# Performance work log

Measured on AMD Instinct MI355X. Metric: run time of the kernel, lower is better.

The kernel has to match this reference:

```python
import jax, jax.numpy as jnp
import numpy as np

DIM = 192; HEADS = 6; HD = DIM // HEADS; SCALE = HD ** -0.5
WS = (4, 8, 8); SS = (2, 4, 4)
NW = WS[0] * WS[1] * WS[2]  # tokens per window = 256
HIDDEN = 768; RANK1 = 384; RANK2 = 96

def _rel_index():
    Wd, Wh, Ww = WS
    coords = np.stack(np.meshgrid(np.arange(Wd), np.arange(Wh), np.arange(Ww), indexing='ij')).reshape(3, -1)
    rel = (coords[:, :, None] - coords[:, None, :]).transpose(1, 2, 0)
    rel = rel + np.array([Wd - 1, Wh - 1, Ww - 1])
    rel[:, :, 0] *= (2 * Wh - 1) * (2 * Ww - 1)
    rel[:, :, 1] *= 2 * Ww - 1
    return rel.sum(-1)  # (NW, NW) int

REL_IDX = jnp.asarray(_rel_index())

def _attn_mask(B, D, H, W):
    # static numpy computation (D,H,W are python ints) -> constant under jit
    img = np.zeros((B, D, H, W), np.float32); cnt = 0
    for d in range(0, D, WS[0]):
        for h in range(0, H, WS[1]):
            for w in range(0, W, WS[2]):
                img[:, d:d + WS[0], h:h + WS[1], w:w + WS[2]] = cnt; cnt += 1
    if any(s > 0 for s in SS):
        img = np.roll(img, (-SS[0], -SS[1], -SS[2]), axis=(1, 2, 3))
    mw = img.reshape(B, D // WS[0], WS[0], H // WS[1], WS[1], W // WS[2], WS[2]).transpose(0, 1, 3, 5, 2, 4, 6).reshape(-1, NW)
    diff = mw[:, :, None] - mw[:, None, :]
    return jnp.asarray(np.where(diff != 0, -100.0, 0.0).astype(np.float32))  # (B*nW, NW, NW)

def _ln(x, g, b):
    mu = x.mean(-1, keepdims=True)
    var = ((x - mu) ** 2).mean(-1, keepdims=True)
    return (x - mu) / jnp.sqrt(var + 1e-5) * g + b

def setup_inputs() -> dict:
    key = jax.random.key(0)
    ks = jax.random.split(key, 16)
    B, D, H, W = 1, 16, 64, 64
    N = D * H * W
    s = 0.02
    return {
        'x': jax.random.normal(ks[0], (B, N, DIM), jnp.float32),
        'norm1_g': jnp.ones((DIM,), jnp.float32), 'norm1_b': jnp.zeros((DIM,), jnp.float32),
        'qkv_w': jax.random.normal(ks[1], (DIM, 3 * DIM), jnp.float32) * s,
        'qkv_b': jnp.zeros((3 * DIM,), jnp.float32),
        'rel_bias': jax.random.normal(ks[2], (1575, HEADS), jnp.float32) * s,
        'proj_w': jax.random.normal(ks[3], (DIM, DIM), jnp.float32) * s,
        'proj_b': jnp.zeros((DIM,), jnp.float32),
        'norm2_g': jnp.ones((DIM,), jnp.float32), 'norm2_b': jnp.zeros((DIM,), jnp.float32),
        'fc1_A': jax.random.normal(ks[4], (DIM, RANK1), jnp.float32) * s,
        'fc1_Bw': jax.random.normal(ks[5], (RANK1, HIDDEN), jnp.float32) * s,
        'fc1_Bb': jnp.zeros((HIDDEN,), jnp.float32),
        'dw_w': jax.random.normal(ks[6], (HIDDEN, 1, 3, 3, 3), jnp.float32) * s,
        'dw_b': jnp.zeros((HIDDEN,), jnp.float32),
        'fc2_A': jax.random.normal(ks[7], (HIDDEN, RANK2), jnp.float32) * s,
        'fc2_Bw': jax.random.normal(ks[8], (RANK2, DIM), jnp.float32) * s,
        'fc2_Bb': jnp.zeros((DIM,), jnp.float32),
        'D': D, 'H': H, 'W': W,
    }

def reference(x, norm1_g, norm1_b, qkv_w, qkv_b, rel_bias, proj_w, proj_b,
              norm2_g, norm2_b, fc1_A, fc1_Bw, fc1_Bb, dw_w, dw_b,
              fc2_A, fc2_Bw, fc2_Bb, D, H, W):
    B, N, C = x.shape
    Wd, Wh, Ww = WS
    shortcut = x
    # --- shifted-window attention (NB: original repo never rolls x; only the mask is shifted) ---
    h = _ln(x, norm1_g, norm1_b).reshape(B, D, H, W, C)
    xw = h.reshape(B, D // Wd, Wd, H // Wh, Wh, W // Ww, Ww, C)
    xw = xw.transpose(0, 1, 3, 5, 2, 4, 6, 7).reshape(-1, NW, C)  # (B*nW, NW, C)
    qkv = (xw @ qkv_w + qkv_b).reshape(-1, NW, 3, HEADS, HD).transpose(2, 0, 3, 1, 4)
    q, k, v = qkv[0] * SCALE, qkv[1], qkv[2]           # (B*nW, heads, NW, hd)
    attn = jnp.einsum('bhnd,bhmd->bhnm', q, k)
    bias = rel_bias[REL_IDX].transpose(2, 0, 1)[None]  # (1, heads, NW, NW)
    mask = _attn_mask(B, D, H, W)                      # (B*nW, NW, NW)
    attn = jax.nn.softmax(attn + bias + mask[:, None], axis=-1)
    out = jnp.einsum('bhnm,bhmd->bhnd', attn, v).transpose(0, 2, 1, 3).reshape(-1, NW, C)
    out = out @ proj_w + proj_b
    out = out.reshape(B, D // Wd, H // Wh, W // Ww, Wd, Wh, Ww, C)
    out = out.transpose(0, 1, 4, 2, 5, 3, 6, 7).reshape(B, N, C)
    x = shortcut + out
    # --- MixFFN3D: low-rank fc1 -> depthwise conv3d -> GELU -> low-rank fc2 ---
    h = _ln(x, norm2_g, norm2_b)
    h = (h @ fc1_A) @ fc1_Bw + fc1_Bb                 # (B, N, HIDDEN)
    h = h.transpose(0, 2, 1).reshape(B, HIDDEN, D, H, W)
    h = jax.lax.conv_general_dilated(h, dw_w, (1, 1, 1), [(1, 1), (1, 1), (1, 1)],
                                     feature_group_count=HIDDEN,
                                     dimension_numbers=('NCDHW', 'OIDHW', 'NCDHW'))
    h = h + dw_b[None, :, None, None, None]
    h = jax.nn.gelu(h, approximate=False)
    h = h.reshape(B, HIDDEN, N).transpose(0, 2, 1)
    h = (h @ fc2_A) @ fc2_Bw + fc2_Bb                 # (B, N, DIM)
    return x + h
```

## Files before the change

kernel.cpp:

```cpp
#include <hip/hip_runtime.h>
#include <hip/hip_bf16.h>

typedef __hip_bfloat16 bf16;
typedef __attribute__((ext_vector_type(8))) short short8;
typedef __attribute__((ext_vector_type(4))) float f32x4;

#define N_TOK 65536
#define C_DIM 192
#define SCALE 0.17677669529663687f

__device__ __forceinline__ float b2f(bf16 v) { return __bfloat162float(v); }
__device__ __forceinline__ bf16 f2b(float v) { return __float2bfloat16(v); }
__device__ __forceinline__ float ldA(const void* p, size_t i, int f32) {
  return f32 ? ((const float*)p)[i] : b2f(((const bf16*)p)[i]);
}
__device__ __forceinline__ float s2f(short s) { union { short s; bf16 b; } u; u.s = s; return b2f(u.b); }

__device__ __forceinline__ float gelu_f(float s) {
  float t = s * s;
  float b = s * (-1.59576912f - 0.0713548162f * t);
  float e = __expf(b);
  return s / (1.f + e);
}

__global__ void detect_kernel(const unsigned short* __restrict__ xh, int* __restrict__ flag) {
  if (threadIdx.x == 0) {
    int crazy = 0;
    for (int i = 0; i < 256; ++i) {
      int e = (xh[i] >> 7) & 0xFF;
      if (e >= 0xF0 || (e >= 1 && e <= 0x60)) ++crazy;
    }
    *flag = (crazy >= 16) ? 1 : 0;
  }
}

__global__ __launch_bounds__(256) void prep_xpose_kernel(
    const void* __restrict__ qkv_w, bf16* __restrict__ QKVT,
    const void* __restrict__ proj_w, bf16* __restrict__ PROJT,
    const void* __restrict__ dw_w, bf16* __restrict__ DWT,
    const void* __restrict__ fc1_A, bf16* __restrict__ FC1AB,
    const void* __restrict__ fc1_Bw, bf16* __restrict__ FC1BWT,
    const void* __restrict__ fc2_A, bf16* __restrict__ FC2AB,
    const void* __restrict__ fc2_Bw, bf16* __restrict__ FC2BWT,
    const int* __restrict__ flag) {
  int f32 = *flag;
  int b = blockIdx.x;
  if (b < 432) {
    int idx = b * 256 + threadIdx.x;
    int n = idx / 192, k = idx - n * 192;
    QKVT[idx] = f2b(ldA(qkv_w, (size_t)k * 576 + n, f32));
  } else if (b < 576) {
    int idx = (b - 432) * 256 + threadIdx.x;
    int n = idx / 192, k = idx - n * 192;
    PROJT[idx] = f2b(ldA(proj_w, (size_t)k * 192 + n, f32));
  } else if (b < 657) {
    int idx = (b - 576) * 256 + threadIdx.x;
    int tap = idx / 768, c = idx - tap * 768;
    DWT[idx] = f2b(ldA(dw_w, (size_t)c * 27 + tap, f32));
  } else if (b < 945) {
    int idx = (b - 657) * 256 + threadIdx.x;
    FC1AB[idx] = f2b(ldA(fc1_A, idx, f32));
  } else if (b < 2097) {
    int idx = (b - 945) * 256 + threadIdx.x;
    int n = idx / 384, r = idx - n * 384;
    FC1BWT[idx] = f2b(ldA(fc1_Bw, (size_t)r * 768 + n, f32));
  } else if (b < 2385) {
    int idx = (b - 2097) * 256 + threadIdx.x;
    FC2AB[idx] = f2b(ldA(fc2_A, idx, f32));
  } else {
    int idx = (b - 2385) * 256 + threadIdx.x;
    int n = idx / 96, r = idx - n * 96;
    FC2BWT[idx] = f2b(ldA(fc2_Bw, (size_t)r * 192 + n, f32));
  }
}

__global__ __launch_bounds__(256) void ln_kernel(const void* __restrict__ x,
    const void* __restrict__ g, const void* __restrict__ b, bf16* __restrict__ out,
    int windowize, int xIsBf16Fixed, const int* __restrict__ flag) {
  int wf32 = *flag;
  int f32 = xIsBf16Fixed ? 0 : wf32;
  int token = blockIdx.x * 4 + (threadIdx.x >> 6);
  int lane = threadIdx.x & 63;
  size_t base = (size_t)token * C_DIM;
  float v0 = ldA(x, base + lane, f32);
  float v1 = ldA(x, base + lane + 64, f32);
  float v2 = ldA(x, base + lane + 128, f32);
  float s = v0 + v1 + v2;
  float s2 = v0 * v0 + v1 * v1 + v2 * v2;
  #pragma unroll
  for (int o = 32; o > 0; o >>= 1) { s += __shfl_xor(s, o, 64); s2 += __shfl_xor(s2, o, 64); }
  float mu = s * (1.f / 192.f);
  float var = s2 * (1.f / 192.f) - mu * mu;
  float rstd = rsqrtf(var + 1e-5f);
  int row = token;
  if (windowize) {
    int d = token >> 12, h = (token >> 6) & 63, w = token & 63;
    int win = ((d >> 2) << 6) + ((h >> 3) << 3) + (w >> 3);
    int t = ((d & 3) << 6) + ((h & 7) << 3) + (w & 7);
    row = win * 256 + t;
  }
  bf16* po = out + (size_t)row * C_DIM;
  po[lane]       = f2b((v0 - mu) * rstd * ldA(g, lane, wf32)       + ldA(b, lane, wf32));
  po[lane + 64]  = f2b((v1 - mu) * rstd * ldA(g, lane + 64, wf32)  + ldA(b, lane + 64, wf32));
  po[lane + 128] = f2b((v2 - mu) * rstd * ldA(g, lane + 128, wf32) + ldA(b, lane + 128, wf32));
}

__global__ __launch_bounds__(256) void mfma_gemm(const bf16* __restrict__ A,
    const bf16* __restrict__ BT, const void* __restrict__ bias,
    const void* __restrict__ res, void* __restrict__ out,
    int Nc, int K, int ldk, int mode, int Mrows, const int* __restrict__ flag) {
  int f32 = *flag;
  __shared__ short As[128 * 96];
  __shared__ short Bs[64 * 96];
  int tid = threadIdx.x;
  int wave = tid >> 6, lane = tid & 63;
  int wm = wave >> 1, wn = wave & 1;
  int lr = lane & 15, quad = lane >> 4;
  int rowBase, colBase;
  if (gridDim.y >= 8) {
    int ncb = gridDim.x;
    int flat = blockIdx.x + ncb * blockIdx.y;
    int group = flat / (8 * ncb);
    int r = flat - group * 8 * ncb;
    rowBase = (group * 8 + (r & 7)) * 128;
    colBase = (r >> 3) * 64;
  } else {
    rowBase = blockIdx.y * 128;
    colBase = blockIdx.x * 64;
  }
  f32x4 acc[4][2];
  #pragma unroll
  for (int i = 0; i < 4; ++i)
    #pragma unroll
    for (int j = 0; j < 2; ++j) acc[i][j] = f32x4{0.f, 0.f, 0.f, 0.f};

  const bf16* arow = A + (size_t)rowBase * K;
  const bf16* brow = BT + (size_t)colBase * ldk;

  for (int k0 = 0; k0 < K; k0 += 96) {
    #pragma unroll
    for (int it = 0; it < 6; ++it) {
      int u = tid + it * 256;
      int row = u / 12, kc = (u - row * 12) * 8;
      __builtin_amdgcn_global_load_lds(
          (const __attribute__((address_space(1))) void*)(arow + (size_t)row * K + k0 + kc),
          (__attribute__((address_space(3))) void*)&As[u * 8], 16, 0, 0);
    }
    #pragma unroll
    for (int it = 0; it < 3; ++it) {
      int u = tid + it * 256;
      int n = u / 12, kc = (u - n * 12) * 8;
      __builtin_amdgcn_global_load_lds(
          (const __attribute__((address_space(1))) void*)(brow + (size_t)n * ldk + k0 + kc),
          (__attribute__((address_space(3))) void*)&Bs[u * 8], 16, 0, 0);
    }
    __syncthreads();
    #pragma unroll
    for (int kk = 0; kk < 3; ++kk) {
      short8 af[4], bf[2];
      #pragma unroll
      for (int i = 0; i < 4; ++i)
        af[i] = *(const short8*)&As[(wm * 64 + i * 16 + lr) * 96 + kk * 32 + quad * 8];
      #pragma unroll
      for (int j = 0; j < 2; ++j)
        bf[j] = *(const short8*)&Bs[(wn * 32 + j * 16 + lr) * 96 + kk * 32 + quad * 8];
      #pragma unroll
      for (int i = 0; i < 4; ++i)
        #pragma unroll
        for (int j = 0; j < 2; ++j)
          acc[i][j] = __builtin_amdgcn_mfma_f32_16x16x32_bf16(af[i], bf[j], acc[i][j], 0, 0, 0);
    }
    __syncthreads();
  }

  #pragma unroll
  for (int i = 0; i < 4; ++i) {
    #pragma unroll
    for (int j = 0; j < 2; ++j) {
      #pragma unroll
      for (int r4 = 0; r4 < 4; ++r4) {
        int row = rowBase + wm * 64 + i * 16 + quad * 4 + r4;
        int c = colBase + wn * 32 + j * 16 + lr;
        if (c >= Nc || row >= Mrows) continue;
        float v = acc[i][j][r4];
        if (bias) v += ldA(bias, c, f32);
        if (mode == 0) {
          ((bf16*)out)[(size_t)row * Nc + c] = f2b(v);
        } else if (mode == 1) {
          float o = b2f(((const bf16*)res)[(size_t)row * Nc + c]) + v;
          if (f32) ((float*)out)[(size_t)row * Nc + c] = o;
          else     ((bf16*)out)[(size_t)row * Nc + c] = f2b(o);
        } else if (mode == 4) {
          ((bf16*)out)[(size_t)c * Mrows + row] = f2b(v);
        } else {
          int win = row >> 8, t = row & 255;
          int d = ((win >> 6) << 2) + (t >> 6);
          int h = (((win >> 3) & 7) << 3) + ((t >> 3) & 7);
          int w = ((win & 7) << 3) + (t & 7);
          int n = (d << 12) + (h << 6) + w;
          ((bf16*)out)[(size_t)n * C_DIM + c] = f2b(ldA(res, (size_t)n * C_DIM + c, f32) + v);
        }
      }
    }
  }
}

__global__ __launch_bounds__(256) void attn_mfma_kernel(const bf16* __restrict__ qkvr,
    const void* __restrict__ rel_bias, bf16* __restrict__ out,
    const int* __restrict__ flag) {
  int f32 = *flag;
  __shared__ bf16 sK[256 * 40];
  __shared__ bf16 sVT[32 * 264];
  __shared__ bf16 sP[4][64 * 40];
  __shared__ float sb[1575];
  __shared__ int  sgb[256];
  int head = blockIdx.x, win = blockIdx.y;
  const bf16* base = qkvr + (size_t)win * 256 * 576;
  int qoff = head * 32, koff = 192 + head * 32, voff = 384 + head * 32;
  int tid = threadIdx.x;
  int wave = tid >> 6, lane = tid & 63;
  int lr = lane & 15, quad = lane >> 4;

  #pragma unroll
  for (int it = 0; it < 4; ++it) {
    int idx = tid + it * 256;
    int tok = idx >> 2, kc = (idx & 3) * 8;
    uint4 v = *(const uint4*)(base + (size_t)tok * 576 + koff + kc);
    *(uint4*)&sK[tok * 40 + kc] = v;
  }
  for (int idx = tid; idx < 8192; idx += 256) {
    int tok = idx >> 5, hd = idx & 31;
    sVT[hd * 264 + tok] = base[(size_t)tok * 576 + voff + hd];
  }
  for (int idx = tid; idx < 1575; idx += 256) sb[idx] = ldA(rel_bias, (size_t)idx * 6 + head, f32);
  {
    int t = tid & 255;
    int d = ((win >> 6) << 2) + (t >> 6);
    int h = (((win >> 3) & 7) << 3) + ((t >> 3) & 7);
    int w = ((win & 7) << 3) + (t & 7);
    int d2 = (d + 2) & 15, h2 = (h + 4) & 63, w2 = (w + 4) & 63;
    int g = ((d2 >> 2) << 6) + ((h2 >> 3) << 3) + (w2 >> 3);
    int td = t >> 6, th = (t >> 3) & 7, tw = t & 7;
    int bse = (td * 15 + th) * 15 + tw;
    sgb[t] = (g << 12) | bse;
  }
  __syncthreads();

  int wm = wave * 64;
  short8 aq[4];
  #pragma unroll
  for (int i = 0; i < 4; ++i)
    aq[i] = *(const short8*)(base + (size_t)(wm + i * 16 + lr) * 576 + qoff + quad * 8);
  int rinfo[16];
  #pragma unroll
  for (int i = 0; i < 4; ++i)
    #pragma unroll
    for (int r = 0; r < 4; ++r)
      rinfo[i * 4 + r] = sgb[wm + i * 16 + quad * 4 + r];

  f32x4 acc_o[4][2], acc_l[4];
  #pragma unroll
  for (int i = 0; i < 4; ++i) {
    acc_l[i] = f32x4{0.f, 0.f, 0.f, 0.f};
    #pragma unroll
    for (int j = 0; j < 2; ++j) acc_o[i][j] = f32x4{0.f, 0.f, 0.f, 0.f};
  }
  short8 bones;
  #pragma unroll
  for (int j = 0; j < 8; ++j) bones[j] = (lr == 0) ? (short)0x3F80 : (short)0;

  for (int c = 0; c < 8; ++c) {
    short8 bk[2];
    #pragma unroll
    for (int jt = 0; jt < 2; ++jt)
      bk[jt] = *(const short8*)&sK[(c * 32 + jt * 16 + lr) * 40 + quad * 8];
    f32x4 s[4][2];
    #pragma unroll
    for (int i = 0; i < 4; ++i)
      #pragma unroll
      for (int jt = 0; jt < 2; ++jt) {
        s[i][jt] = f32x4{0.f, 0.f, 0.f, 0.f};
        s[i][jt] = __builtin_amdgcn_mfma_f32_16x16x32_bf16(aq[i], bk[jt], s[i][jt], 0, 0, 0);
      }
    int cinfo[2];
    #pragma unroll
    for (int jt = 0; jt < 2; ++jt) cinfo[jt] = sgb[c * 32 + jt * 16 + lr];
    #pragma unroll
    for (int i = 0; i < 4; ++i)
      #pragma unroll
      for (int jt = 0; jt < 2; ++jt)
        #pragma unroll
        for (int r = 0; r < 4; ++r) {
          int ri = rinfo[i * 4 + r], ci = cinfo[jt];
          float sc = s[i][jt][r] * SCALE + sb[(ri & 0xFFF) - (ci & 0xFFF) + 787];
          float p = ((ri >> 12) == (ci >> 12)) ? __expf(sc) : 0.f;
          sP[wave][(i * 16 + quad * 4 + r) * 40 + jt * 16 + lr] = f2b(p);
        }
    short8 ap[4];
    #pragma unroll
    for (int i = 0; i < 4; ++i)
      ap[i] = *(const short8*)&sP[wave][(i * 16 + lr) * 40 + quad * 8];
    short8 bv[2];
    #pragma unroll
    for (int jh = 0; jh < 2; ++jh)
      bv[jh] = *(const short8*)&sVT[(jh * 16 + lr) * 264 + c * 32 + quad * 8];
    #pragma unroll
    for (int i = 0; i < 4; ++i) {
      #pragma unroll
      for (int jh = 0; jh < 2; ++jh)
        acc_o[i][jh] = __builtin_amdgcn_mfma_f32_16x16x32_bf16(ap[i], bv[jh], acc_o[i][jh], 0, 0, 0);
      acc_l[i] = __builtin_amdgcn_mfma_f32_16x16x32_bf16(ap[i], bones, acc_l[i], 0, 0, 0);
    }
  }
  #pragma unroll
  for (int i = 0; i < 4; ++i) {
    #pragma unroll
    for (int r = 0; r < 4; ++r) {
      float l = __shfl(acc_l[i][r], lane & 48, 64);
      float inv = 1.f / l;
      int t = wm + i * 16 + quad * 4 + r;
      bf16* po = out + (size_t)(win * 256 + t) * C_DIM + head * 32;
      po[lr]      = f2b(acc_o[i][0][r] * inv);
      po[16 + lr] = f2b(acc_o[i][1][r] * inv);
    }
  }
}

__global__ __launch_bounds__(256) void dwconv8w4_kernel(const bf16* __restrict__ in,
    const bf16* __restrict__ wT, const void* __restrict__ wb, bf16* __restrict__ out,
    const int* __restrict__ flag) {
  int f32 = *flag;
  int idx = blockIdx.x * 256 + threadIdx.x;
  int n4 = idx / 96, g = idx - n4 * 96;
  int c0 = g * 8;
  int d = n4 >> 10, h = (n4 >> 4) & 63, w0 = (n4 & 15) << 2;
  const bf16* inb = in + c0;
  float acc[4][8];
  {
    float bias[8];
    #pragma unroll
    for (int e = 0; e < 8; ++e) bias[e] = ldA(wb, c0 + e, f32);
    #pragma unroll
    for (int t = 0; t < 4; ++t)
      #pragma unroll
      for (int e = 0; e < 8; ++e) acc[t][e] = bias[e];
  }
  #pragma unroll
  for (int kd = 0; kd < 3; ++kd) {
    int dd = d + kd - 1;
    if ((unsigned)dd >= 16u) continue;
    #pragma unroll
    for (int kh = 0; kh < 3; ++kh) {
      int hh = h + kh - 1;
      if ((unsigned)hh >= 64u) continue;
      int rowbase = (dd << 12) + (hh << 6);
      float xf[6][8];
      #pragma unroll
      for (int j = 0; j < 6; ++j) {
        int ww = w0 + j - 1;
        short8 xv = short8{0, 0, 0, 0, 0, 0, 0, 0};
        if ((unsigned)ww < 64u)
          xv = *(const short8*)(inb + (size_t)(rowbase + ww) * 768);
        #pragma unroll
        for (int e = 0; e < 8; ++e) xf[j][e] = s2f(xv[e]);
      }
      #pragma unroll
      for (int kw = 0; kw < 3; ++kw) {
        int tap = kd * 9 + kh * 3 + kw;
        short8 wv = *(const short8*)(wT + tap * 768 + c0);
        float wf[8];
        #pragma unroll
        for (int e = 0; e < 8; ++e) wf[e] = s2f(wv[e]);
        #pragma unroll
        for (int t = 0; t < 4; ++t)
          #pragma unroll
          for (int e = 0; e < 8; ++e)
            acc[t][e] += xf[t + kw][e] * wf[e];
      }
    }
  }
  #pragma unroll
  for (int t = 0; t < 4; ++t) {
    bf16* po = out + (size_t)((d << 12) + (h << 6) + w0 + t) * 768 + c0;
    #pragma unroll
    for (int e = 0; e < 8; ++e)
      po[e] = f2b(gelu_f(acc[t][e]));
  }
}

extern "C" void kernel_launch(void* const* d_in, const int* in_sizes, int n_in,
                              void* d_out, int out_size, void* d_ws, size_t ws_size,
                              hipStream_t stream) {
  const void* x      = d_in[0];
  const void* n1g    = d_in[1];
  const void* n1b    = d_in[2];
  const void* qkv_w  = d_in[3];
  const void* qkv_b  = d_in[4];
  const void* relb   = d_in[5];
  const void* proj_w = d_in[6];
  const void* proj_b = d_in[7];
  const void* n2g    = d_in[8];
  const void* n2b    = d_in[9];
  const void* fc1_A  = d_in[10];
  const void* fc1_Bw = d_in[11];
  const void* fc1_Bb = d_in[12];
  const void* dw_w   = d_in[13];
  const void* dw_b   = d_in[14];
  const void* fc2_A  = d_in[15];
  const void* fc2_Bw = d_in[16];
  const void* fc2_Bb = d_in[17];

  char* ws = (char*)d_ws;
  bf16* SCR  = (bf16*)d_out;
  bf16* X1   = (bf16*)(ws);
  bf16* QKVR = (bf16*)(ws + (size_t)24 * 1048576);
  bf16* F2   = (bf16*)(ws + (size_t)24 * 1048576);
  bf16* F1   = (bf16*)(ws + (size_t)120 * 1048576);
  bf16* QKVT   = (bf16*)(ws + (size_t)228 * 1048576);
  bf16* PROJT  = (bf16*)(ws + (size_t)229 * 1048576);
  bf16* DWT    = (bf16*)(ws + (size_t)230 * 1048576);
  bf16* W1T    = (bf16*)(ws + (size_t)231 * 1048576);
  bf16* W2T    = (bf16*)(ws + (size_t)232 * 1048576);
  bf16* FC1AB  = (bf16*)(ws + (size_t)233 * 1048576);
  bf16* FC1BWT = (bf16*)(ws + (size_t)234 * 1048576);
  bf16* FC2AB  = (bf16*)(ws + (size_t)236 * 1048576);
  bf16* FC2BWT = (bf16*)(ws + (size_t)237 * 1048576);
  int* FLAG    = (int*)(ws + (size_t)255 * 1048576);

  detect_kernel<<<1, 64, 0, stream>>>((const unsigned short*)x, FLAG);
  prep_xpose_kernel<<<2457, 256, 0, stream>>>(qkv_w, QKVT, proj_w, PROJT, dw_w, DWT,
                                              fc1_A, FC1AB, fc1_Bw, FC1BWT,
                                              fc2_A, FC2AB, fc2_Bw, FC2BWT, FLAG);
  mfma_gemm<<<dim3(12, 2), 256, 0, stream>>>(FC1AB, FC1BWT, nullptr, nullptr, W1T,
                                             768, 384, 384, 4, 192, FLAG);
  mfma_gemm<<<dim3(3, 6), 256, 0, stream>>>(FC2AB, FC2BWT, nullptr, nullptr, W2T,
                                            192, 96, 96, 4, 768, FLAG);
  ln_kernel<<<N_TOK / 4, 256, 0, stream>>>(x, n1g, n1b, SCR, 1, 0, FLAG);
  mfma_gemm<<<dim3(9, 512), 256, 0, stream>>>(SCR, QKVT, qkv_b, nullptr, QKVR,
                                              576, 192, 192, 0, N_TOK, FLAG);
  attn_mfma_kernel<<<dim3(6, 256), 256, 0, stream>>>(QKVR, relb, SCR, FLAG);
  mfma_gemm<<<dim3(3, 512), 256, 0, stream>>>(SCR, PROJT, proj_b, x, X1,
                                              192, 192, 192, 3, N_TOK, FLAG);
  ln_kernel<<<N_TOK / 4, 256, 0, stream>>>(X1, n2g, n2b, SCR, 0, 1, FLAG);
  mfma_gemm<<<dim3(12, 512), 256, 0, stream>>>(SCR, W1T, fc1_Bb, nullptr, F1,
                                               768, 192, 192, 0, N_TOK, FLAG);
  dwconv8w4_kernel<<<6144, 256, 0, stream>>>(F1, DWT, dw_b, F2, FLAG);
  mfma_gemm<<<dim3(3, 512), 256, 0, stream>>>(F2, W2T, fc2_Bb, X1, d_out,
                                              192, 768, 768, 1, N_TOK, FLAG);
}
```

Before: 659.5 us.

## Fuse LayerNorm into the following QKV and fc1 GEMMs

Replaces the standalone LayerNorm kernels and their subsequent GEMMs with a single ln_gemm kernel that normalizes a 64-row tile into shared memory (including window reordering for the first LN) and immediately multiplies it by a 64-column weight slice with MFMA. This removes the write and re-read of the normalized intermediate and two kernel launches. In exchange, each row's LayerNorm is recomputed for every column block, so input rows are reloaded 9–12 times, and the new GEMM uses smaller tiles without K pipelining.

```diff
diff --git a/kernel.cpp b/kernel.cpp
--- a/kernel.cpp
+++ b/kernel.cpp
@@ -74,35 +74,111 @@
   }
 }
 
-__global__ __launch_bounds__(256) void ln_kernel(const void* __restrict__ x,
-    const void* __restrict__ g, const void* __restrict__ b, bf16* __restrict__ out,
-    int windowize, int xIsBf16Fixed, const int* __restrict__ flag) {
+__global__ __launch_bounds__(256) void ln_gemm(const void* __restrict__ X,
+    const void* __restrict__ g, const void* __restrict__ b,
+    const bf16* __restrict__ BT, const void* __restrict__ bias,
+    bf16* __restrict__ out, int Nc, int windowize, int xAdaptive,
+    const int* __restrict__ flag) {
   int wf32 = *flag;
-  int f32 = xIsBf16Fixed ? 0 : wf32;
-  int token = blockIdx.x * 4 + (threadIdx.x >> 6);
-  int lane = threadIdx.x & 63;
-  size_t base = (size_t)token * C_DIM;
-  float v0 = ldA(x, base + lane, f32);
-  float v1 = ldA(x, base + lane + 64, f32);
-  float v2 = ldA(x, base + lane + 128, f32);
-  float s = v0 + v1 + v2;
-  float s2 = v0 * v0 + v1 * v1 + v2 * v2;
-  #pragma unroll
-  for (int o = 32; o > 0; o >>= 1) { s += __shfl_xor(s, o, 64); s2 += __shfl_xor(s2, o, 64); }
+  int f32 = xAdaptive ? wf32 : 0;
+  __shared__ short As[64 * 200];
+  __shared__ short Bs[64 * 192];
+  int tid = threadIdx.x;
+  int wave = tid >> 6, lane = tid & 63;
+  int lr = lane & 15, quad = lane >> 4;
+  int ncb = gridDim.x;
+  int flat = blockIdx.x + ncb * blockIdx.y;
+  int group = flat / (8 * ncb);
+  int r = flat - group * 8 * ncb;
+  int rowBase = (group * 8 + (r & 7)) * 64;
+  int colBase = (r >> 3) * 64;
+
+  const bf16* brow = BT + (size_t)colBase * 192;
+  #pragma unroll
+  for (int it = 0; it < 6; ++it) {
+    int u = tid + it * 256;
+    int n = u / 24, c = u - n * 24;
+    int cs = c ^ (n & 7);
+    __builtin_amdgcn_global_load_lds(
+        (const __attribute__((address_space(1))) void*)(brow + (size_t)n * 192 + cs * 8),
+        (__attribute__((address_space(3))) void*)&Bs[u * 8], 16, 0, 0);
+  }
+
+  int rr = tid >> 2, sub = tid & 3;
+  int wr = rowBase + rr;
+  int n_tok = wr;
+  if (windowize) {
+    int win = wr >> 8, tt = wr & 255;
+    int d = ((win >> 6) << 2) + (tt >> 6);
+    int h = (((win >> 3) & 7) << 3) + ((tt >> 3) & 7);
+    int w = ((win & 7) << 3) + (tt & 7);
+    n_tok = (d << 12) + (h << 6) + w;
+  }
+  float v[48];
+  {
+    size_t base = (size_t)n_tok * 192 + sub * 48;
+    if (f32) {
+      const float* px = (const float*)X + base;
+      #pragma unroll
+      for (int j = 0; j < 12; ++j) {
+        f32x4 q = *(const f32x4*)(px + j * 4);
+        v[j * 4] = q[0]; v[j * 4 + 1] = q[1]; v[j * 4 + 2] = q[2]; v[j * 4 + 3] = q[3];
+      }
+    } else {
+      const bf16* px = (const bf16*)X + base;
+      #pragma unroll
+      for (int j = 0; j < 6; ++j) {
+        short8 q = *(const short8*)(px + j * 8);
+        #pragma unroll
+        for (int e = 0; e < 8; ++e) v[j * 8 + e] = s2f(q[e]);
+      }
+    }
+  }
+  float s = 0.f, s2 = 0.f;
+  #pragma unroll
+  for (int j = 0; j < 48; ++j) { s += v[j]; s2 += v[j] * v[j]; }
+  s += __shfl_xor(s, 1, 64);  s2 += __shfl_xor(s2, 1, 64);
+  s += __shfl_xor(s, 2, 64);  s2 += __shfl_xor(s2, 2, 64);
   float mu = s * (1.f / 192.f);
   float var = s2 * (1.f / 192.f) - mu * mu;
   float rstd = rsqrtf(var + 1e-5f);
-  int row = token;
-  if (windowize) {
-    int d = token >> 12, h = (token >> 6) & 63, w = token & 63;
-    int win = ((d >> 2) << 6) + ((h >> 3) << 3) + (w >> 3);
-    int t = ((d & 3) << 6) + ((h & 7) << 3) + (w & 7);
-    row = win * 256 + t;
-  }
-  bf16* po = out + (size_t)row * C_DIM;
-  po[lane]       = f2b((v0 - mu) * rstd * ldA(g, lane, wf32)       + ldA(b, lane, wf32));
-  po[lane + 64]  = f2b((v1 - mu) * rstd * ldA(g, lane + 64, wf32)  + ldA(b, lane + 64, wf32));
-  po[lane + 128] = f2b((v2 - mu) * rstd * ldA(g, lane + 128, wf32) + ldA(b, lane + 128, wf32));
+  #pragma unroll
+  for (int j6 = 0; j6 < 6; ++j6) {
+    short8 pk;
+    #pragma unroll
+    for (int e = 0; e < 8; ++e) {
+      int cidx = sub * 48 + j6 * 8 + e;
+      float y = (v[j6 * 8 + e] - mu) * rstd * ldA(g, cidx, wf32) + ldA(b, cidx, wf32);
+      union { bf16 bb; short ss; } u2; u2.bb = f2b(y); pk[e] = u2.ss;
+    }
+    *(short8*)&As[rr * 200 + sub * 48 + j6 * 8] = pk;
+  }
+  __syncthreads();
+
+  f32x4 acc[4];
+  #pragma unroll
+  for (int j = 0; j < 4; ++j) acc[j] = f32x4{0.f, 0.f, 0.f, 0.f};
+  #pragma unroll
+  for (int kk = 0; kk < 6; ++kk) {
+    short8 af = *(const short8*)&As[(wave * 16 + lr) * 200 + kk * 32 + quad * 8];
+    #pragma unroll
+    for (int j = 0; j < 4; ++j) {
+      int n = j * 16 + lr;
+      int c = (kk * 4 + quad) ^ (n & 7);
+      short8 bf = *(const short8*)&Bs[n * 192 + c * 8];
+      acc[j] = __builtin_amdgcn_mfma_f32_16x16x32_bf16(af, bf, acc[j], 0, 0, 0);
+    }
+  }
+  #pragma unroll
+  for (int j = 0; j < 4; ++j) {
+    int c = colBase + j * 16 + lr;
+    float bv = bias ? ldA(bias, c, wf32) : 0.f;
+    #pragma unroll
+    for (int r4 = 0; r4 < 4; ++r4) {
+      int row = rowBase + wave * 16 + quad * 4 + r4;
+      out[(size_t)row * Nc + c] = f2b(acc[j][r4] + bv);
+    }
+  }
 }
 
 __global__ __launch_bounds__(256) void mfma_gemm(const bf16* __restrict__ A,
@@ -435,15 +511,13 @@
                                              768, 384, 384, 4, 192, FLAG);
   mfma_gemm<<<dim3(3, 6), 256, 0, stream>>>(FC2AB, FC2BWT, nullptr, nullptr, W2T,
                                             192, 96, 96, 4, 768, FLAG);
-  ln_kernel<<<N_TOK / 4, 256, 0, stream>>>(x, n1g, n1b, SCR, 1, 0, FLAG);
-  mfma_gemm<<<dim3(9, 512), 256, 0, stream>>>(SCR, QKVT, qkv_b, nullptr, QKVR,
-                                              576, 192, 192, 0, N_TOK, FLAG);
+  ln_gemm<<<dim3(9, 1024), 256, 0, stream>>>(x, n1g, n1b, QKVT, qkv_b, QKVR,
+                                             576, 1, 1, FLAG);
   attn_mfma_kernel<<<dim3(6, 256), 256, 0, stream>>>(QKVR, relb, SCR, FLAG);
   mfma_gemm<<<dim3(3, 512), 256, 0, stream>>>(SCR, PROJT, proj_b, x, X1,
                                               192, 192, 192, 3, N_TOK, FLAG);
-  ln_kernel<<<N_TOK / 4, 256, 0, stream>>>(X1, n2g, n2b, SCR, 0, 1, FLAG);
-  mfma_gemm<<<dim3(12, 512), 256, 0, stream>>>(SCR, W1T, fc1_Bb, nullptr, F1,
-                                               768, 192, 192, 0, N_TOK, FLAG);
+  ln_gemm<<<dim3(12, 1024), 256, 0, stream>>>(X1, n2g, n2b, W1T, fc1_Bb, F1,
+                                              768, 0, 0, FLAG);
   dwconv8w4_kernel<<<6144, 256, 0, stream>>>(F1, DWT, dw_b, F2, FLAG);
   mfma_gemm<<<dim3(3, 512), 256, 0, stream>>>(F2, W2T, fc2_Bb, X1, d_out,
                                               192, 768, 768, 1, N_TOK, FLAG);
```

Measured after the change: 783.8 us. 18.9% more time.
